# Performance work log

Measured on AMD Instinct MI355X. Metric: run time of the kernel, lower is better.

Reference implementation:

```python
import jax, jax.numpy as jnp
import numpy as np
from jax import lax

NPOINT = 1024   # number of FPS centroids (init kwarg npoint)
NSAMPLE = 32    # neighbors per group (init kwarg nsample); radius is unused in the source
B, N, D = 8, 4096, 64


def setup_inputs() -> dict:
    key = jax.random.key(0)
    k1, k2, k3 = jax.random.split(key, 3)
    xyz = jax.random.normal(k1, (B, 3, N), dtype=jnp.float32)
    points = jax.random.normal(k2, (B, D, N), dtype=jnp.float32)
    farthest_init = jax.random.randint(k3, (B,), 0, N)
    return {"xyz": xyz, "points": points, "farthest_init": farthest_init}


def _fps(x, farthest_init, npoint):
    # x: [B,N,3] -> centroid indices [B,npoint]. Sequential argmax/min-update, like the torch loop.
    b, n, _ = x.shape
    bidx = jnp.arange(b)

    def step(carry, _):
        dist, far = carry                      # dist: [B,N], far: [B]
        centroid = x[bidx, far]                # [B,3]
        d = jnp.sum((x - centroid[:, None, :]) ** 2, -1)
        dist = jnp.minimum(dist, d)            # == masked update dist[mask]=d[mask]
        return (dist, jnp.argmax(dist, -1)), far

    init = (jnp.full((b, n), 1e10, dtype=x.dtype), farthest_init)
    _, cent = lax.scan(step, init, None, length=npoint)
    return cent.T                              # [B,npoint]


def _forward(xyz, points, farthest_init):
    x = xyz.transpose(0, 2, 1)                 # [B,N,3]
    p = points.transpose(0, 2, 1)              # [B,N,D]
    b = x.shape[0]
    bidx = jnp.arange(b)

    # FPS indices are non-differentiable (long tensor in torch) -> stop_gradient
    fps_idx = _fps(lax.stop_gradient(x), farthest_init, NPOINT)   # [B,S]
    new_xyz = x[bidx[:, None], fps_idx]        # [B,S,3]

    # pairwise squared distances [B,S,N] (same expansion as square_distance)
    sq = (jnp.sum(new_xyz ** 2, -1)[:, :, None]
          + jnp.sum(x ** 2, -1)[:, None, :]
          - 2.0 * jnp.einsum('bsc,bnc->bsn', new_xyz, x))
    # source sorts and takes first nsample == nsample smallest distances
    _, idx = lax.top_k(-lax.stop_gradient(sq), NSAMPLE)           # [B,S,K]

    g_xyz = x[bidx[:, None, None], idx]        # [B,S,K,3]
    g_pts = p[bidx[:, None, None], idx]        # [B,S,K,D]
    new_points = jnp.concatenate([g_xyz, g_pts], -1)              # [B,S,K,3+D]

    # permute(0,3,2,1) then max over dim 2 == max over K then transpose
    feat = jnp.max(new_points, axis=2).transpose(0, 2, 1)         # [B,3+D,S]
    return new_xyz.transpose(0, 2, 1), feat                       # [B,3,S], [B,3+D,S]


def reference(xyz, points, farthest_init):
    return _forward(xyz, points, farthest_init)
```

## Files before the change

kernel.cpp:

```cpp
#include <hip/hip_runtime.h>

#define BB 8
#define NN 4096
#define DD 64
#define SS 1024
#define KK 32
#define GINF 1e30f

__device__ __forceinline__ float fmulrn(float a, float b){ return __fmul_rn(a,b); }
__device__ __forceinline__ float faddrn(float a, float b){ return __fadd_rn(a,b); }
__device__ __forceinline__ float fsubrn(float a, float b){ return __fsub_rn(a,b); }

template<int CTRL>
__device__ __forceinline__ float dpp_fmax(float v){
  int o = __builtin_amdgcn_update_dpp(0, __float_as_int(v), CTRL, 0xf, 0xf, true);
  return fmaxf(v, __int_as_float(o));
}

__global__ __launch_bounds__(256) void sqx_kernel(const float* __restrict__ xyz,
                                                  float* __restrict__ sqx){
  int i = blockIdx.x * 256 + threadIdx.x;
  int b = i >> 12, n = i & (NN - 1);
  const float* xb = xyz + b * 3 * NN;
  float x = xb[n], y = xb[NN + n], z = xb[2 * NN + n];
  sqx[i] = faddrn(faddrn(fmulrn(x, x), fmulrn(y, y)), fmulrn(z, z));
}

__global__ __launch_bounds__(512) void fps_kernel(const float* __restrict__ xyz,
                                                  const int* __restrict__ finit,
                                                  int* __restrict__ fps_idx){
  __shared__ float4 sc[2][8];
  __shared__ int    sn[2][8];
  int b = blockIdx.x, tid = threadIdx.x;
  int lane = tid & 63, w = tid >> 6;
  const float* xb = xyz + b * 3 * NN;
  float px[8], py[8], pz[8], dist[8];
  int nbase = tid << 3;
  #pragma unroll
  for (int j = 0; j < 8; ++j){
    px[j] = xb[nbase + j];
    py[j] = xb[NN + nbase + j];
    pz[j] = xb[2 * NN + nbase + j];
    dist[j] = 1e10f;
  }
  int far = finit[b];
  float cx = xb[far], cy = xb[NN + far], cz = xb[2 * NN + far];
  if (tid == 0) fps_idx[b * SS] = far;

  for (int it = 0; it < SS - 1; ++it){
    float lm = 0.0f;
    #pragma unroll
    for (int j = 0; j < 8; ++j){
      float tx = fsubrn(px[j], cx), ty = fsubrn(py[j], cy), tz = fsubrn(pz[j], cz);
      float d2 = faddrn(faddrn(fmulrn(tx, tx), fmulrn(ty, ty)), fmulrn(tz, tz));
      float dk = fminf(dist[j], d2);
      dist[j] = dk;
      lm = fmaxf(lm, dk);
    }
    float v = lm;
    v = dpp_fmax<0x111>(v);
    v = dpp_fmax<0x112>(v);
    v = dpp_fmax<0x114>(v);
    v = dpp_fmax<0x118>(v);
    v = dpp_fmax<0x142>(v);
    v = dpp_fmax<0x143>(v);
    float maxv = __int_as_float(__builtin_amdgcn_readlane(__float_as_int(v), 63));
    int loc = 8;
    float scx = 0.f, scy = 0.f, scz = 0.f;
    #pragma unroll
    for (int j = 7; j >= 0; --j){
      if (dist[j] == maxv){ loc = j; scx = px[j]; scy = py[j]; scz = pz[j]; }
    }
    unsigned long long bal = __ballot(loc < 8);
    int fl = __ffsll(bal) - 1;
    int par = it & 1;
    if (lane == fl){
      sc[par][w] = make_float4(scx, scy, scz, maxv);
      sn[par][w] = nbase + loc;
    }
    __syncthreads();
    float4 s0 = sc[par][0]; int n0 = sn[par][0];
    #pragma unroll
    for (int q = 1; q < 8; ++q){
      float4 sq_ = sc[par][q]; int nq = sn[par][q];
      if (sq_.w > s0.w || (sq_.w == s0.w && nq < n0)){ s0 = sq_; n0 = nq; }
    }
    cx = s0.x; cy = s0.y; cz = s0.z; far = n0;
    if (tid == 0) fps_idx[b * SS + it + 1] = far;
  }
}

__global__ __launch_bounds__(256) void knn_kernel(const float* __restrict__ xyz,
                                                  const float* __restrict__ points,
                                                  const float* __restrict__ sqx,
                                                  const int* __restrict__ fps_idx,
                                                  float* __restrict__ out){
  __shared__ int nbr[4][KK];
  int tid = threadIdx.x;
  int lane = tid & 63, wslot = tid >> 6;
  int gw = blockIdx.x * 4 + wslot;
  int b = gw >> 10, cs = gw & 1023;
  const float* xb = xyz + b * 3 * NN;
  const float* sb = sqx + b * NN;
  int c0 = fps_idx[b * SS + cs];
  float cx = xb[c0], cy = xb[NN + c0], cz = xb[2 * NN + c0];
  float sqc = sb[c0];

  float d[64];
  #pragma unroll
  for (int k = 0; k < 64; ++k){
    int n = (k << 6) | lane;
    float xn = xb[n], yn = xb[NN + n], zn = xb[2 * NN + n], sn = sb[n];
    float dot = faddrn(faddrn(fmulrn(cx, xn), fmulrn(cy, yn)), fmulrn(cz, zn));
    d[k] = fsubrn(faddrn(sqc, sn), fmulrn(2.0f, dot));
  }

  float gv[8]; int gn[8];
  #pragma unroll
  for (int j = 0; j < 8; ++j){
    float nv = GINF; int nn2 = 0x40000000;
    #pragma unroll
    for (int t = 0; t < 8; ++t){
      int k = j * 8 + t; int n = (k << 6) | lane;
      if (d[k] < nv){ nv = d[k]; nn2 = n; }
    }
    gv[j] = nv; gn[j] = nn2;
  }

  float lv = -GINF; int ln = -1;
  for (int r = 0; r < KK; ++r){
    float bv = gv[0]; int bn = gn[0];
    #pragma unroll
    for (int j = 1; j < 8; ++j){ if (gv[j] < bv){ bv = gv[j]; bn = gn[j]; } }
    #pragma unroll
    for (int m = 1; m < 64; m <<= 1){
      float ov = __shfl_xor(bv, m);
      int   on = __shfl_xor(bn, m);
      if (ov < bv || (ov == bv && on < bn)){ bv = ov; bn = on; }
    }
    if (lane == 0) nbr[wslot][r] = bn;
    lv = bv; ln = bn;
    int jsel = __builtin_amdgcn_readfirstlane(bn >> 9);
    #define RECOMP(J) if (jsel == (J)) { float nv = GINF; int nn2 = 0x40000000; \
      _Pragma("unroll") \
      for (int t = 0; t < 8; ++t){ int k = (J) * 8 + t; int n = (k << 6) | lane; \
        bool pass = (d[k] > lv) || (d[k] == lv && n > ln); \
        if (pass && d[k] < nv){ nv = d[k]; nn2 = n; } } \
      gv[(J)] = nv; gn[(J)] = nn2; }
    RECOMP(0) RECOMP(1) RECOMP(2) RECOMP(3)
    RECOMP(4) RECOMP(5) RECOMP(6) RECOMP(7)
    #undef RECOMP
  }
  __syncthreads();

  const float* pb = points + b * DD * NN;
  float fm = -GINF, xm = -GINF, ym = -GINF, zm = -GINF;
  #pragma unroll 8
  for (int j = 0; j < KK; ++j){
    int nj = nbr[wslot][j];
    fm = fmaxf(fm, pb[lane * NN + nj]);
    xm = fmaxf(xm, xb[nj]);
    ym = fmaxf(ym, xb[NN + nj]);
    zm = fmaxf(zm, xb[2 * NN + nj]);
  }
  float* out1 = out + BB * 3 * SS;
  float* o1b  = out1 + b * 67 * SS;
  o1b[(3 + lane) * SS + cs] = fm;
  if (lane == 0){
    o1b[cs] = xm; o1b[SS + cs] = ym; o1b[2 * SS + cs] = zm;
    float* o0b = out + b * 3 * SS;
    o0b[cs] = cx; o0b[SS + cs] = cy; o0b[2 * SS + cs] = cz;
  }
}

extern "C" void kernel_launch(void* const* d_in, const int* in_sizes, int n_in,
                              void* d_out, int out_size, void* d_ws, size_t ws_size,
                              hipStream_t stream){
  const float* xyz    = (const float*)d_in[0];
  const float* points = (const float*)d_in[1];
  const int*   finit  = (const int*)d_in[2];
  float* out = (float*)d_out;
  int*   fps_idx = (int*)d_ws;
  float* sqx     = (float*)((char*)d_ws + BB * SS * sizeof(int));

  hipLaunchKernelGGL(sqx_kernel, dim3(BB * NN / 256), dim3(256), 0, stream, xyz, sqx);
  hipLaunchKernelGGL(fps_kernel, dim3(BB), dim3(512), 0, stream, xyz, finit, fps_idx);
  hipLaunchKernelGGL(knn_kernel, dim3(BB * SS / 4), dim3(256), 0, stream,
                     xyz, points, sqx, fps_idx, out);
}
```

Measured before the change: 1.359 ms.

## Run FPS in a single wavefront with packed FP32 math and no block barriers

Result: slower. 1.903 ms (+40.1%).

```diff
diff --git a/kernel.cpp b/kernel.cpp
--- a/kernel.cpp
+++ b/kernel.cpp
@@ -7,14 +7,27 @@
 #define KK 32
 #define GINF 1e30f
 
+typedef float f32x2 __attribute__((ext_vector_type(2)));
+
 __device__ __forceinline__ float fmulrn(float a, float b){ return __fmul_rn(a,b); }
 __device__ __forceinline__ float faddrn(float a, float b){ return __fadd_rn(a,b); }
 __device__ __forceinline__ float fsubrn(float a, float b){ return __fsub_rn(a,b); }
+
+__device__ __forceinline__ f32x2 pk_add(f32x2 a, f32x2 b){
+  f32x2 d; asm("v_pk_add_f32 %0, %1, %2" : "=v"(d) : "v"(a), "v"(b)); return d;
+}
+__device__ __forceinline__ f32x2 pk_mul(f32x2 a, f32x2 b){
+  f32x2 d; asm("v_pk_mul_f32 %0, %1, %2" : "=v"(d) : "v"(a), "v"(b)); return d;
+}
 
 template<int CTRL>
 __device__ __forceinline__ float dpp_fmax(float v){
   int o = __builtin_amdgcn_update_dpp(0, __float_as_int(v), CTRL, 0xf, 0xf, true);
   return fmaxf(v, __int_as_float(o));
+}
+
+__device__ __forceinline__ float fneg_exact(float c){
+  return __int_as_float(__float_as_int(c) ^ 0x80000000);
 }
 
 __global__ __launch_bounds__(256) void sqx_kernel(const float* __restrict__ xyz,
@@ -26,37 +39,61 @@
   sqx[i] = faddrn(faddrn(fmulrn(x, x), fmulrn(y, y)), fmulrn(z, z));
 }
 
-__global__ __launch_bounds__(512) void fps_kernel(const float* __restrict__ xyz,
-                                                  const int* __restrict__ finit,
-                                                  int* __restrict__ fps_idx){
-  __shared__ float4 sc[2][8];
-  __shared__ int    sn[2][8];
-  int b = blockIdx.x, tid = threadIdx.x;
-  int lane = tid & 63, w = tid >> 6;
+__global__ __launch_bounds__(64) void fps_kernel(const float* __restrict__ xyz,
+                                                 const int* __restrict__ finit,
+                                                 int* __restrict__ fps_idx){
+  __shared__ float lx[NN], ly[NN], lz[NN];
+  int b = blockIdx.x, lane = threadIdx.x;
   const float* xb = xyz + b * 3 * NN;
-  float px[8], py[8], pz[8], dist[8];
-  int nbase = tid << 3;
+  for (int k = lane; k < NN; k += 64){
+    lx[k] = xb[k]; ly[k] = xb[NN + k]; lz[k] = xb[2 * NN + k];
+  }
+  f32x2 px[32], py[32], pz[32], dd[32];
+  const float* xr = xb + (lane << 6);
   #pragma unroll
-  for (int j = 0; j < 8; ++j){
-    px[j] = xb[nbase + j];
-    py[j] = xb[NN + nbase + j];
-    pz[j] = xb[2 * NN + nbase + j];
-    dist[j] = 1e10f;
+  for (int p = 0; p < 32; ++p){
+    px[p] = *(const f32x2*)(xr + 2 * p);
+    py[p] = *(const f32x2*)(xr + NN + 2 * p);
+    pz[p] = *(const f32x2*)(xr + 2 * NN + 2 * p);
+    dd[p] = (f32x2){1e10f, 1e10f};
   }
   int far = finit[b];
   float cx = xb[far], cy = xb[NN + far], cz = xb[2 * NN + far];
-  if (tid == 0) fps_idx[b * SS] = far;
+  if (lane == 0) fps_idx[b * SS] = far;
+  __syncthreads();
 
   for (int it = 0; it < SS - 1; ++it){
-    float lm = 0.0f;
-    #pragma unroll
-    for (int j = 0; j < 8; ++j){
-      float tx = fsubrn(px[j], cx), ty = fsubrn(py[j], cy), tz = fsubrn(pz[j], cz);
-      float d2 = faddrn(faddrn(fmulrn(tx, tx), fmulrn(ty, ty)), fmulrn(tz, tz));
-      float dk = fminf(dist[j], d2);
-      dist[j] = dk;
-      lm = fmaxf(lm, dk);
-    }
+    f32x2 ncx = {fneg_exact(cx), fneg_exact(cx)};
+    f32x2 ncy = {fneg_exact(cy), fneg_exact(cy)};
+    f32x2 ncz = {fneg_exact(cz), fneg_exact(cz)};
+    float ga[8] = {0.f,0.f,0.f,0.f,0.f,0.f,0.f,0.f};
+    #pragma unroll
+    for (int p = 0; p < 32; ++p){
+      f32x2 tx = pk_add(px[p], ncx);
+      f32x2 ty = pk_add(py[p], ncy);
+      f32x2 tz = pk_add(pz[p], ncz);
+      f32x2 d2 = pk_add(pk_add(pk_mul(tx, tx), pk_mul(ty, ty)), pk_mul(tz, tz));
+      dd[p].x = fminf(dd[p].x, d2.x);
+      dd[p].y = fminf(dd[p].y, d2.y);
+      ga[p >> 2] = fmaxf(ga[p >> 2], fmaxf(dd[p].x, dd[p].y));
+    }
+    float lm = fmaxf(fmaxf(fmaxf(ga[0], ga[1]), fmaxf(ga[2], ga[3])),
+                     fmaxf(fmaxf(ga[4], ga[5]), fmaxf(ga[6], ga[7])));
+    int loc[8];
+    #pragma unroll
+    for (int c = 0; c < 8; ++c){
+      int l = -1;
+      #pragma unroll
+      for (int t = 7; t >= 0; --t){
+        int j = c * 8 + t, p = j >> 1;
+        float dv = (j & 1) ? dd[p].y : dd[p].x;
+        if (dv == lm) l = j;
+      }
+      loc[c] = l;
+    }
+    int jloc = -1;
+    #pragma unroll
+    for (int c = 7; c >= 0; --c) if (loc[c] >= 0) jloc = loc[c];
     float v = lm;
     v = dpp_fmax<0x111>(v);
     v = dpp_fmax<0x112>(v);
@@ -65,28 +102,12 @@
     v = dpp_fmax<0x142>(v);
     v = dpp_fmax<0x143>(v);
     float maxv = __int_as_float(__builtin_amdgcn_readlane(__float_as_int(v), 63));
-    int loc = 8;
-    float scx = 0.f, scy = 0.f, scz = 0.f;
-    #pragma unroll
-    for (int j = 7; j >= 0; --j){
-      if (dist[j] == maxv){ loc = j; scx = px[j]; scy = py[j]; scz = pz[j]; }
-    }
-    unsigned long long bal = __ballot(loc < 8);
+    unsigned long long bal = __ballot(lm == maxv);
     int fl = __ffsll(bal) - 1;
-    int par = it & 1;
-    if (lane == fl){
-      sc[par][w] = make_float4(scx, scy, scz, maxv);
-      sn[par][w] = nbase + loc;
-    }
-    __syncthreads();
-    float4 s0 = sc[par][0]; int n0 = sn[par][0];
-    #pragma unroll
-    for (int q = 1; q < 8; ++q){
-      float4 sq_ = sc[par][q]; int nq = sn[par][q];
-      if (sq_.w > s0.w || (sq_.w == s0.w && nq < n0)){ s0 = sq_; n0 = nq; }
-    }
-    cx = s0.x; cy = s0.y; cz = s0.z; far = n0;
-    if (tid == 0) fps_idx[b * SS + it + 1] = far;
+    int n_cand = (lane << 6) + jloc;
+    int n0 = __builtin_amdgcn_readlane(n_cand, fl);
+    cx = lx[n0]; cy = ly[n0]; cz = lz[n0];
+    if (lane == 0) fps_idx[b * SS + it + 1] = n0;
   }
 }
 
@@ -184,7 +205,7 @@
   float* sqx     = (float*)((char*)d_ws + BB * SS * sizeof(int));
 
   hipLaunchKernelGGL(sqx_kernel, dim3(BB * NN / 256), dim3(256), 0, stream, xyz, sqx);
-  hipLaunchKernelGGL(fps_kernel, dim3(BB), dim3(512), 0, stream, xyz, finit, fps_idx);
+  hipLaunchKernelGGL(fps_kernel, dim3(BB), dim3(64), 0, stream, xyz, finit, fps_idx);
   hipLaunchKernelGGL(knn_kernel, dim3(BB * SS / 4), dim3(256), 0, stream,
                      xyz, points, sqx, fps_idx, out);
 }
```
